# Performance work log

Measured on AMD Instinct MI355X. Metric: run time of the kernel, lower is better.

## Reference

```python
import jax, jax.numpy as jnp
import numpy as np

HIDDEN = 2048
N_HEADS = 16
N_KV_HEADS = 4
HEAD_DIM = 128
N_REP = N_HEADS // N_KV_HEADS
BATCH = 2
SEQ = 2048
SCALE = HEAD_DIM ** -0.5
NEG = -1e9


def apply_rope(x, freqs):
    # x: (b, s, h, d); freqs: (s, d//2) angles. Interleaved-pair rotation.
    cos = jnp.cos(freqs)[None, :, None, :]
    sin = jnp.sin(freqs)[None, :, None, :]
    x1 = x[..., 0::2]
    x2 = x[..., 1::2]
    r1 = x1 * cos - x2 * sin
    r2 = x1 * sin + x2 * cos
    return jnp.stack([r1, r2], axis=-1).reshape(x.shape)


def setup_inputs() -> dict:
    key = jax.random.key(0)
    ks = jax.random.split(key, 6)
    x = jax.random.normal(ks[0], (BATCH, SEQ, HIDDEN), dtype=jnp.float32)
    wq = jax.random.normal(ks[1], (N_HEADS * HEAD_DIM, HIDDEN), dtype=jnp.float32) * 0.02
    wk = jax.random.normal(ks[2], (N_KV_HEADS * HEAD_DIM, HIDDEN), dtype=jnp.float32) * 0.02
    wv = jax.random.normal(ks[3], (N_KV_HEADS * HEAD_DIM, HIDDEN), dtype=jnp.float32) * 0.02
    wo = jax.random.normal(ks[4], (HIDDEN, N_HEADS * HEAD_DIM), dtype=jnp.float32) * 0.02
    # RoPE angle table: pos * theta^{-2i/d}
    inv_freq = 1.0 / (10000.0 ** (jnp.arange(0, HEAD_DIM, 2, dtype=jnp.float32) / HEAD_DIM))
    rope_freqs = jnp.arange(SEQ, dtype=jnp.float32)[:, None] * inv_freq[None, :]  # (S, d/2)
    # additive causal mask
    causal = jnp.tril(jnp.ones((SEQ, SEQ), dtype=bool))
    mask = jnp.where(causal, 0.0, NEG).astype(jnp.float32)[None, None]  # (1,1,S,S)
    return {"x": x, "wq": wq, "wk": wk, "wv": wv, "wo": wo,
            "rope_freqs": rope_freqs, "mask": mask}


def reference(x, wq, wk, wv, wo, rope_freqs, mask):
    b, s, _ = x.shape
    q = (x @ wq.T).reshape(b, s, N_HEADS, HEAD_DIM)
    k = (x @ wk.T).reshape(b, s, N_KV_HEADS, HEAD_DIM)
    v = (x @ wv.T).reshape(b, s, N_KV_HEADS, HEAD_DIM)
    q = apply_rope(q, rope_freqs)
    k = apply_rope(k, rope_freqs)
    new_k, new_v = k, v  # kv cache (no prior cache, start_pos=0)
    # GQA: repeat each kv head n_rep times (matches expand+reshape in source)
    k_rep = jnp.repeat(k, N_REP, axis=2)  # (b, s, n_heads, d)
    v_rep = jnp.repeat(v, N_REP, axis=2)
    scores = jnp.einsum('bqhd,bkhd->bhqk', q, k_rep) * SCALE
    scores = scores + mask
    attn = jax.nn.softmax(scores.astype(jnp.float32), axis=-1).astype(q.dtype)
    out = jnp.einsum('bhqk,bkhd->bqhd', attn, v_rep).reshape(b, s, -1)
    return out @ wo.T, (new_k, new_v)
```

## Files before the change

### kernel.cpp

```cpp
#include <hip/hip_runtime.h>
#include <hip/hip_bf16.h>

#define NH 16
#define NKV 4
#define HD 128
#define QSCALE 0.1275174272f

using bf16x8 = __attribute__((ext_vector_type(8))) __bf16;
using f32x4  = __attribute__((ext_vector_type(4))) float;
using u16x8  = __attribute__((ext_vector_type(8))) unsigned short;
using u16x4  = __attribute__((ext_vector_type(4))) unsigned short;
using u16x2  = __attribute__((ext_vector_type(2))) unsigned short;

__device__ __forceinline__ unsigned short f2b(float f) {
  __hip_bfloat16 h = __float2bfloat16(f);
  return __builtin_bit_cast(unsigned short, h);
}
__device__ __forceinline__ float b2f(unsigned short u) {
  unsigned int v = ((unsigned int)u) << 16;
  return __builtin_bit_cast(float, v);
}

__device__ __forceinline__ void glds16(const unsigned short* g, unsigned short* l) {
  __builtin_amdgcn_global_load_lds(
      (const __attribute__((address_space(1))) unsigned int*)(const void*)g,
      (__attribute__((address_space(3))) unsigned int*)(void*)l, 16, 0, 0);
}

__global__ __launch_bounds__(256) void cvt_fused(const float* __restrict__ x,
                                                 const float* __restrict__ wq,
                                                 const float* __restrict__ wk,
                                                 const float* __restrict__ wv,
                                                 const float* __restrict__ wo,
                                                 const float* __restrict__ freqs,
                                                 unsigned short* __restrict__ xb,
                                                 unsigned short* __restrict__ wqkvb,
                                                 unsigned short* __restrict__ wob,
                                                 float2* __restrict__ cs_tab) {
  int i = blockIdx.x * 256 + threadIdx.x;
  if (i >= 2359296) {
    int k = i - 2359296;
    float f = freqs[k];
    float2 cs; cs.x = cosf(f); cs.y = sinf(f);
    cs_tab[k] = cs;
    return;
  }
  const float* src;
  unsigned short* dst;
  int off;
  if (i < 1048576)      { src = x;  dst = xb;              off = i; }
  else if (i < 1572864) { src = wq; dst = wqkvb;           off = i - 1048576; }
  else if (i < 1703936) { src = wk; dst = wqkvb + 4194304; off = i - 1572864; }
  else if (i < 1835008) { src = wv; dst = wqkvb + 5242880; off = i - 1703936; }
  else                  { src = wo; dst = wob;             off = i - 1835008; }
  const float4* s4 = reinterpret_cast<const float4*>(src) + (size_t)off * 2;
  float4 v0 = s4[0], v1 = s4[1];
  u16x8 o;
  o[0] = f2b(v0.x); o[1] = f2b(v0.y); o[2] = f2b(v0.z); o[3] = f2b(v0.w);
  o[4] = f2b(v1.x); o[5] = f2b(v1.y); o[6] = f2b(v1.z); o[7] = f2b(v1.w);
  reinterpret_cast<u16x8*>(dst)[off] = o;
}

__global__ __launch_bounds__(512, 1) void gemm_qkv(const unsigned short* __restrict__ A,
                                                   const unsigned short* __restrict__ B,
                                                   const float2* __restrict__ cs_tab,
                                                   unsigned short* __restrict__ qro,
                                                   unsigned short* __restrict__ kro,
                                                   unsigned short* __restrict__ vt,
                                                   float* __restrict__ newk,
                                                   float* __restrict__ newv,
                                                   int K) {
  constexpr int BN = 384;
  constexpr int AF = 4, BF = 6, BH = 3, BL = 3;
  __shared__ unsigned short As[3][128 * 32];
  __shared__ unsigned short Bs[3][BN * 32];
  const int tid = threadIdx.x, lane = tid & 63;
  const int wid = tid >> 6, wm = wid >> 2, wn = wid & 3;
  const int cpx = gridDim.x >> 3;
  const int wgid = (blockIdx.x & 7) * cpx + (blockIdx.x >> 3);
  const int bx = wgid % 8, by = wgid / 8;
  const int row0 = by * 128, col0 = bx * BN;
  const int fr = lane & 15, g = lane >> 4;
  const int NT = K >> 5;

  size_t offA;
  {
    int cid = tid, R = cid >> 3, phys = cid & 7, cl = phys ^ (R & 7);
    offA = (size_t)(row0 + 2 * R + (cl >> 2)) * K + (cl & 3) * 8;
  }
  size_t offB[BL];
#pragma unroll
  for (int l = 0; l < BL; l++) {
    int cid = tid + l * 512, R = cid >> 3, phys = cid & 7, cl = phys ^ (R & 7);
    offB[l] = (size_t)(col0 + 2 * R + (cl >> 2)) * K + (cl & 3) * 8;
  }

  auto stage_p0 = [&](int t, int sb) {
    int k0 = t * 32;
    glds16(A + offA + k0, &As[sb][tid * 8]);
    glds16(B + offB[0] + k0, &Bs[sb][tid * 8]);
  };
  auto stage_p1 = [&](int t, int sb) {
    int k0 = t * 32;
#pragma unroll
    for (int l = 1; l < BL; l++)
      glds16(B + offB[l] + k0, &Bs[sb][(tid + l * 512) * 8]);
  };

  auto ldfrag = [&](const unsigned short* buf, int row) {
    int R = row >> 1;
    int phys = ((((row & 1) << 2) | g) ^ (R & 7));
    return *reinterpret_cast<const bf16x8*>(&buf[R * 64 + phys * 8]);
  };

  f32x4 acc[AF][BF];
#pragma unroll
  for (int i = 0; i < AF; i++)
#pragma unroll
    for (int j = 0; j < BF; j++) acc[i][j] = f32x4{0.f, 0.f, 0.f, 0.f};

  stage_p0(0, 0); stage_p1(0, 0);
  stage_p0(1, 1); stage_p1(1, 1);
  asm volatile("s_waitcnt vmcnt(4)" ::: "memory");
  __builtin_amdgcn_s_barrier();
  __builtin_amdgcn_sched_barrier(0);

  int rb = 0, sb = 2;
#pragma unroll 1
  for (int t = 0; t < NT; ++t) {
    const unsigned short* Ar = &As[rb][0];
    const unsigned short* Br = &Bs[rb][0];

    bf16x8 af[AF], bfr[BF];
#pragma unroll
    for (int mf = 0; mf < AF; mf++) af[mf] = ldfrag(Ar, wm * 64 + mf * 16 + fr);
#pragma unroll
    for (int nf = 0; nf < BH; nf++) bfr[nf] = ldfrag(Br, wn * 96 + nf * 16 + fr);
    if (t + 2 < NT) stage_p0(t + 2, sb);
    __builtin_amdgcn_s_barrier();
    asm volatile("s_waitcnt lgkmcnt(0)" ::: "memory");
    __builtin_amdgcn_sched_barrier(0);
    __builtin_amdgcn_s_setprio(1);
#pragma unroll
    for (int mf = 0; mf < AF; mf++)
#pragma unroll
      for (int nf = 0; nf < BH; nf++)
        acc[mf][nf] = __builtin_amdgcn_mfma_f32_16x16x32_bf16(af[mf], bfr[nf], acc[mf][nf], 0, 0, 0);
    __builtin_amdgcn_s_setprio(0);
    __builtin_amdgcn_sched_barrier(0);
    __builtin_amdgcn_s_barrier();

#pragma unroll
    for (int nf = BH; nf < BF; nf++) bfr[nf] = ldfrag(Br, wn * 96 + nf * 16 + fr);
    if (t + 2 < NT) stage_p1(t + 2, sb);
    __builtin_amdgcn_s_barrier();
    asm volatile("s_waitcnt lgkmcnt(0)" ::: "memory");
    __builtin_amdgcn_sched_barrier(0);
    __builtin_amdgcn_s_setprio(1);
#pragma unroll
    for (int mf = 0; mf < AF; mf++)
#pragma unroll
      for (int nf = BH; nf < BF; nf++)
        acc[mf][nf] = __builtin_amdgcn_mfma_f32_16x16x32_bf16(af[mf], bfr[nf], acc[mf][nf], 0, 0, 0);
    __builtin_amdgcn_s_setprio(0);
    __builtin_amdgcn_sched_barrier(0);

    if (t + 1 < NT) {
      if (t + 2 < NT) asm volatile("s_waitcnt vmcnt(4)" ::: "memory");
      else            asm volatile("s_waitcnt vmcnt(0)" ::: "memory");
      __builtin_amdgcn_s_barrier();
      __builtin_amdgcn_sched_barrier(0);
    }
    rb = rb == 2 ? 0 : rb + 1;
    sb = sb == 2 ? 0 : sb + 1;
  }

#pragma unroll
  for (int i = 0; i < AF; i++) {
    int rbase = row0 + wm * 64 + i * 16 + g * 4;
    int bb = rbase >> 11;
    int sr0 = rbase & 2047;
#pragma unroll
    for (int j = 0; j < BF; j++) {
      int cb = col0 + wn * 96 + j * 16 + fr;
      int d = cb & 127;
      if (cb < 2048) {
        int hq = cb >> 7;
        unsigned short* qp = qro + ((size_t)(bb * 16 + hq) * 2048 + sr0) * 128 + d;
#pragma unroll
        for (int r = 0; r < 4; r++) {
          float own = acc[i][j][r];
          float par = __shfl_xor(own, 1);
          float2 cs = cs_tab[(sr0 + r) * 64 + (d >> 1)];
          float o = (fr & 1) ? (par * cs.y + own * cs.x) : (own * cs.x - par * cs.y);
          qp[(size_t)r * 128] = f2b(o * QSCALE);
        }
      } else if (cb < 2560) {
        int kvh = (cb >> 7) & 3;
        unsigned short* kp = kro + ((size_t)(bb * 4 + kvh) * 2048 + sr0) * 128 + d;
        float* nk = newk + ((size_t)bb * 2048 + sr0) * 512 + kvh * 128 + d;
#pragma unroll
        for (int r = 0; r < 4; r++) {
          float own = acc[i][j][r];
          float par = __shfl_xor(own, 1);
          float2 cs = cs_tab[(sr0 + r) * 64 + (d >> 1)];
          float o = (fr & 1) ? (par * cs.y + own * cs.x) : (own * cs.x - par * cs.y);
          kp[(size_t)r * 128] = f2b(o);
          nk[(size_t)r * 512] = o;
        }
      } else {
        int kvh = (cb >> 7) & 3;
        float* nv = newv + ((size_t)bb * 2048 + sr0) * 512 + kvh * 128 + d;
        u16x4 pack;
#pragma unroll
        for (int r = 0; r < 4; r++) {
          float v = acc[i][j][r];
          nv[(size_t)r * 512] = v;
          pack[r] = f2b(v);
        }
        int kl = sr0 & 31;
        int slotb = ((kl >> 2) & 3) * 8 + (kl >> 4) * 4;
        *reinterpret_cast<u16x4*>(vt + ((size_t)(bb * 4 + kvh) * 128 + d) * 2048
                                  + (sr0 & ~31) + slotb) = pack;
      }
    }
  }
}

template<int CF32, int BN>
__global__ __launch_bounds__(512, 1) void gemm_full(const unsigned short* __restrict__ A,
                                                    const unsigned short* __restrict__ B,
                                                    void* __restrict__ C,
                                                    int N, int K, int nbx) {
  constexpr int BM = 128;
  constexpr int AF = 4;
  constexpr int BF = BN / 64;
  constexpr int BH = BF / 2;
  constexpr int AL = 1;
  constexpr int BL = BN / 128;
  __shared__ unsigned short As[3][BM * 32];
  __shared__ unsigned short Bs[3][BN * 32];
  const int tid = threadIdx.x, lane = tid & 63;
  const int wid = tid >> 6, wm = wid >> 2, wn = wid & 3;
  const int cpx = gridDim.x >> 3;
  const int wgid = (blockIdx.x & 7) * cpx + (blockIdx.x >> 3);
  const int bx = wgid % nbx, by = wgid / nbx;
  const int row0 = by * BM, col0 = bx * BN;
  const int fr = lane & 15, g = lane >> 4;
  const int NT = K >> 5;

  size_t offA;
  {
    int cid = tid, R = cid >> 3, phys = cid & 7, cl = phys ^ (R & 7);
    offA = (size_t)(row0 + 2 * R + (cl >> 2)) * K + (cl & 3) * 8;
  }
  size_t offB[BL];
#pragma unroll
  for (int l = 0; l < BL; l++) {
    int cid = tid + l * 512, R = cid >> 3, phys = cid & 7, cl = phys ^ (R & 7);
    offB[l] = (size_t)(col0 + 2 * R + (cl >> 2)) * K + (cl & 3) * 8;
  }

  auto stage_p0 = [&](int t, int sb) {
    int k0 = t * 32;
    glds16(A + offA + k0, &As[sb][tid * 8]);
    glds16(B + offB[0] + k0, &Bs[sb][tid * 8]);
  };
  auto stage_p1 = [&](int t, int sb) {
    int k0 = t * 32;
#pragma unroll
    for (int l = 1; l < BL; l++)
      glds16(B + offB[l] + k0, &Bs[sb][(tid + l * 512) * 8]);
  };

  auto ldfrag = [&](const unsigned short* buf, int row) {
    int R = row >> 1;
    int phys = ((((row & 1) << 2) | g) ^ (R & 7));
    return *reinterpret_cast<const bf16x8*>(&buf[R * 64 + phys * 8]);
  };

  f32x4 acc[AF][BF];
#pragma unroll
  for (int i = 0; i < AF; i++)
#pragma unroll
    for (int j = 0; j < BF; j++) acc[i][j] = f32x4{0.f, 0.f, 0.f, 0.f};

  stage_p0(0, 0); stage_p1(0, 0);
  stage_p0(1, 1); stage_p1(1, 1);
  if constexpr (AL + BL == 4) asm volatile("s_waitcnt vmcnt(4)" ::: "memory");
  else                        asm volatile("s_waitcnt vmcnt(3)" ::: "memory");
  __builtin_amdgcn_s_barrier();
  __builtin_amdgcn_sched_barrier(0);

  int rb = 0, sb = 2;
#pragma unroll 1
  for (int t = 0; t < NT; ++t) {
    const unsigned short* Ar = &As[rb][0];
    const unsigned short* Br = &Bs[rb][0];

    bf16x8 af[AF], bfr[BF];
#pragma unroll
    for (int mf = 0; mf < AF; mf++) af[mf] = ldfrag(Ar, wm * 64 + mf * 16 + fr);
#pragma unroll
    for (int nf = 0; nf < BH; nf++) bfr[nf] = ldfrag(Br, wn * (BN / 4) + nf * 16 + fr);
    if (t + 2 < NT) stage_p0(t + 2, sb);
    __builtin_amdgcn_s_barrier();
    asm volatile("s_waitcnt lgkmcnt(0)" ::: "memory");
    __builtin_amdgcn_sched_barrier(0);
    __builtin_amdgcn_s_setprio(1);
#pragma unroll
    for (int mf = 0; mf < AF; mf++)
#pragma unroll
      for (int nf = 0; nf < BH; nf++)
        acc[mf][nf] = __builtin_amdgcn_mfma_f32_16x16x32_bf16(af[mf], bfr[nf], acc[mf][nf], 0, 0, 0);
    __builtin_amdgcn_s_setprio(0);
    __builtin_amdgcn_sched_barrier(0);
    __builtin_amdgcn_s_barrier();

#pragma unroll
    for (int nf = BH; nf < BF; nf++) bfr[nf] = ldfrag(Br, wn * (BN / 4) + nf * 16 + fr);
    if (t + 2 < NT) stage_p1(t + 2, sb);
    __builtin_amdgcn_s_barrier();
    asm volatile("s_waitcnt lgkmcnt(0)" ::: "memory");
    __builtin_amdgcn_sched_barrier(0);
    __builtin_amdgcn_s_setprio(1);
#pragma unroll
    for (int mf = 0; mf < AF; mf++)
#pragma unroll
      for (int nf = BH; nf < BF; nf++)
        acc[mf][nf] = __builtin_amdgcn_mfma_f32_16x16x32_bf16(af[mf], bfr[nf], acc[mf][nf], 0, 0, 0);
    __builtin_amdgcn_s_setprio(0);
    __builtin_amdgcn_sched_barrier(0);

    if (t + 1 < NT) {
      if (t + 2 < NT) {
        if constexpr (AL + BL == 4) asm volatile("s_waitcnt vmcnt(4)" ::: "memory");
        else                        asm volatile("s_waitcnt vmcnt(3)" ::: "memory");
      } else {
        asm volatile("s_waitcnt vmcnt(0)" ::: "memory");
      }
      __builtin_amdgcn_s_barrier();
      __builtin_amdgcn_sched_barrier(0);
    }
    rb = rb == 2 ? 0 : rb + 1;
    sb = sb == 2 ? 0 : sb + 1;
  }

#pragma unroll
  for (int i = 0; i < AF; i++) {
#pragma unroll
    for (int j = 0; j < BF; j++) {
      int rbase = row0 + wm * 64 + i * 16 + g * 4;
      int cb = col0 + wn * (BN / 4) + j * 16 + fr;
#pragma unroll
      for (int r = 0; r < 4; r++) {
        if (CF32)
          reinterpret_cast<float*>(C)[(size_t)(rbase + r) * N + cb] = acc[i][j][r];
        else
          reinterpret_cast<unsigned short*>(C)[(size_t)(rbase + r) * N + cb] = f2b(acc[i][j][r]);
      }
    }
  }
}

__global__ __launch_bounds__(512, 4) void attn_kernel(const unsigned short* __restrict__ qro,
                                                      const unsigned short* __restrict__ kro,
                                                      const unsigned short* __restrict__ vt,
                                                      unsigned short* __restrict__ out) {
  __shared__ unsigned short Ks[2][32 * 128];
  __shared__ unsigned short Vs[2][64 * 64];
  const int tid = threadIdx.x, lane = tid & 63, w = tid >> 6;
  const int kvhb = blockIdx.x & 7;
  const int kvh = kvhb & 3, b = kvhb >> 2;
  const int s = blockIdx.x >> 3;
  const int T = (s < 32) ? s : (95 - s);
  const int sub = w >> 2, hh = w & 3;
  const int h = kvh * 4 + hh;
  const int qbase = T * 32 + sub * 16;
  const int fr = lane & 15, g = lane >> 4, fk = g * 8;
  const unsigned short* Kp = kro + (size_t)(b * 4 + kvh) * 2048 * 128;
  const unsigned short* Vtp = vt + (size_t)(b * 4 + kvh) * 128 * 2048;
  const unsigned short* Qp = qro + ((size_t)(b * 16 + h) * 2048 + qbase) * 128;

  bf16x8 qf[4];
#pragma unroll
  for (int kk = 0; kk < 4; kk++)
    qf[kk] = *reinterpret_cast<const bf16x8*>(Qp + fr * 128 + kk * 32 + fk);

  u16x8 onesu;
#pragma unroll
  for (int j = 0; j < 8; j++) onesu[j] = 0x3F80;
  bf16x8 ones = __builtin_bit_cast(bf16x8, onesu);

  f32x4 o[8];
#pragma unroll
  for (int dt = 0; dt < 8; dt++) o[dt] = f32x4{0.f, 0.f, 0.f, 0.f};
  f32x4 dacc = f32x4{0.f, 0.f, 0.f, 0.f};
  const int qrow_s = qbase + fr;
  const int niter = T + 1;

  const int krow = w * 4 + (lane >> 4);
  const int kcol = lane & 15;
  const int vr = w * 8 + (lane >> 3);
  const int vcol = lane & 7;

  auto stage = [&](int kv0, int buf) {
    glds16(Kp + (size_t)(kv0 + krow) * 128 + ((kcol ^ (krow & 7)) * 8),
           &Ks[buf][w * 4 * 128]);
    int u = vcol ^ (vr & 7);
    int d = 2 * vr + (u >> 2);
    glds16(Vtp + (size_t)d * 2048 + kv0 + (u & 3) * 8,
           &Vs[buf][w * 8 * 64]);
  };

  auto step = [&](int kv0, bool mask, int buf) {
    const unsigned short* Kb = &Ks[buf][0];
    const unsigned short* Vb = &Vs[buf][0];
    f32x4 sc[2];
    sc[0] = sc[1] = f32x4{0.f, 0.f, 0.f, 0.f};
    __builtin_amdgcn_s_setprio(1);
#pragma unroll
    for (int kk = 0; kk < 4; kk++) {
      int blk = ((kk * 4 + g) ^ (fr & 7)) * 8;
      bf16x8 ka0 = *reinterpret_cast<const bf16x8*>(Kb + (fr +  0) * 128 + blk);
      bf16x8 ka1 = *reinterpret_cast<const bf16x8*>(Kb + (fr + 16) * 128 + blk);
      sc[0] = __builtin_amdgcn_mfma_f32_16x16x32_bf16(ka0, qf[kk], sc[0], 0, 0, 0);
      sc[1] = __builtin_amdgcn_mfma_f32_16x16x32_bf16(ka1, qf[kk], sc[1], 0, 0, 0);
    }
    __builtin_amdgcn_s_setprio(0);
#pragma unroll
    for (int ss = 0; ss < 2; ss++)
#pragma unroll
      for (int r = 0; r < 4; r++) {
        float v = sc[ss][r];
        if (mask && (kv0 + 16 * ss + 4 * g + r > qrow_s)) v = -1e30f;
        sc[ss][r] = __builtin_amdgcn_exp2f(v);
      }
    u16x8 pau;
#pragma unroll
    for (int j = 0; j < 4; j++) {
      pau[j]     = f2b(sc[0][j]);
      pau[4 + j] = f2b(sc[1][j]);
    }
    bf16x8 pa = __builtin_bit_cast(bf16x8, pau);
    dacc = __builtin_amdgcn_mfma_f32_16x16x32_bf16(pa, ones, dacc, 0, 0, 0);
    __builtin_amdgcn_s_setprio(1);
#pragma unroll
    for (int dt = 0; dt < 8; dt++) {
      int jr = dt * 8 + (fr >> 1);
      int c = ((fr & 1) * 4 + g) ^ (fr >> 1);
      bf16x8 vf = *reinterpret_cast<const bf16x8*>(Vb + jr * 64 + c * 8);
      o[dt] = __builtin_amdgcn_mfma_f32_16x16x32_bf16(pa, vf, o[dt], 0, 0, 0);
    }
    __builtin_amdgcn_s_setprio(0);
  };

  stage(0, 0);
  int buf = 0;
  for (int i = 0; i < niter; i++) {
    __syncthreads();
    if (i + 1 < niter) stage((i + 1) * 32, buf ^ 1);
    step(i * 32, i == niter - 1, buf);
    buf ^= 1;
  }

#pragma unroll
  for (int r = 0; r < 4; r++) {
    float inv = 1.0f / dacc[r];
    int qrow = qbase + g * 4 + r;
    size_t rowoff = ((size_t)b * 2048 + qrow) * 2048 + (size_t)h * 128;
#pragma unroll
    for (int dt = 0; dt < 8; dt++)
      out[rowoff + dt * 16 + fr] = f2b(o[dt][r] * inv);
  }
}

extern "C" void kernel_launch(void* const* d_in, const int* in_sizes, int n_in,
                              void* d_out, int out_size, void* d_ws, size_t ws_size,
                              hipStream_t stream) {
  const float* x  = (const float*)d_in[0];
  const float* wq = (const float*)d_in[1];
  const float* wk = (const float*)d_in[2];
  const float* wv = (const float*)d_in[3];
  const float* wo = (const float*)d_in[4];
  const float* freqs = (const float*)d_in[5];

  char* ws = (char*)d_ws;
  unsigned short* xb    = (unsigned short*)(ws);
  unsigned short* attn  = xb;
  unsigned short* wqkvb = (unsigned short*)(ws + 16777216);
  unsigned short* wob   = (unsigned short*)(ws + 29360128);
  float2*         cstab = (float2*)(ws + 37748736);
  unsigned short* qro   = (unsigned short*)(ws + 62914560);
  unsigned short* kro   = (unsigned short*)(ws + 79691776);
  unsigned short* vt    = (unsigned short*)(ws + 83886080);

  float* out_o = (float*)d_out;
  float* out_k = (float*)d_out + 8388608;
  float* out_v = (float*)d_out + 10485760;

  cvt_fused<<<9728, 256, 0, stream>>>(x, wq, wk, wv, wo, freqs, xb, wqkvb, wob, cstab);

  gemm_qkv<<<256, 512, 0, stream>>>(xb, wqkvb, cstab, qro, kro, vt, out_k, out_v, 2048);

  attn_kernel<<<512, 512, 0, stream>>>(qro, kro, vt, attn);

  gemm_full<1, 256><<<256, 512, 0, stream>>>(attn, wob, out_o, 2048, 2048, 8);
}
```

Baseline: 195.4 us.

## Replace large-tile triple-buffered GEMMs with 128x128 double-buffered tiles and more blocks

Both the QKV projection and output projection GEMMs drop their 128x384/128x256 tiles with 512 threads, triple buffering and hand-tuned waitcnt/barrier splitting. They now use 128x128 tiles with 256 threads, simple double buffering and __syncthreads, launching 768 and 512 blocks with up to 3 blocks per CU. The aim is higher occupancy and better CU load balance across the grid. In exchange, per-block operand reuse drops, the finer-grained latency hiding schedule is gone, and more global traffic is needed per output.

Measured after the change: 193.1 us. About the same (-1.2%).

```diff
diff --git a/kernel.cpp b/kernel.cpp
--- a/kernel.cpp
+++ b/kernel.cpp
@@ -61,7 +61,31 @@
   reinterpret_cast<u16x8*>(dst)[off] = o;
 }
 
-__global__ __launch_bounds__(512, 1) void gemm_qkv(const unsigned short* __restrict__ A,
+
+#define GEMM97_PREAMBLE(Kvar)                                                  \
+  const int tid = threadIdx.x, lane = tid & 63;                                \
+  const int wid = tid >> 6, wm = wid >> 1, wn = wid & 1;                       \
+  const int cpx = gridDim.x >> 3;                                              \
+  const int wgid = (blockIdx.x & 7) * cpx + (blockIdx.x >> 3);                 \
+  const int bx = wgid % nbx, by = wgid / nbx;                                  \
+  const int row0 = by * 128, col0 = bx * 128;                                  \
+  const int fr = lane & 15, g = lane >> 4;                                     \
+  const int NT = (Kvar) >> 5;                                                  \
+  size_t offA[2], offB[2];                                                     \
+  _Pragma("unroll")                                                            \
+  for (int l = 0; l < 2; l++) {                                                \
+    int cid = tid + l * 256, R = cid >> 3, phys = cid & 7, cl = phys ^ (R & 7);\
+    offA[l] = (size_t)(row0 + 2 * R + (cl >> 2)) * (Kvar) + (cl & 3) * 8;      \
+    offB[l] = (size_t)(col0 + 2 * R + (cl >> 2)) * (Kvar) + (cl & 3) * 8;      \
+  }
+
+__device__ __forceinline__ bf16x8 ldfrag97(const unsigned short* buf, int row, int g) {
+  int R = row >> 1;
+  int phys = ((((row & 1) << 2) | g) ^ (R & 7));
+  return *reinterpret_cast<const bf16x8*>(&buf[R * 64 + phys * 8]);
+}
+
+__global__ __launch_bounds__(256, 3) void gemm_qkv(const unsigned short* __restrict__ A,
                                                    const unsigned short* __restrict__ B,
                                                    const float2* __restrict__ cs_tab,
                                                    unsigned short* __restrict__ qro,
@@ -69,120 +93,55 @@
                                                    unsigned short* __restrict__ vt,
                                                    float* __restrict__ newk,
                                                    float* __restrict__ newv,
-                                                   int K) {
-  constexpr int BN = 384;
-  constexpr int AF = 4, BF = 6, BH = 3, BL = 3;
-  __shared__ unsigned short As[3][128 * 32];
-  __shared__ unsigned short Bs[3][BN * 32];
-  const int tid = threadIdx.x, lane = tid & 63;
-  const int wid = tid >> 6, wm = wid >> 2, wn = wid & 3;
-  const int cpx = gridDim.x >> 3;
-  const int wgid = (blockIdx.x & 7) * cpx + (blockIdx.x >> 3);
-  const int bx = wgid % 8, by = wgid / 8;
-  const int row0 = by * 128, col0 = bx * BN;
-  const int fr = lane & 15, g = lane >> 4;
-  const int NT = K >> 5;
-
-  size_t offA;
-  {
-    int cid = tid, R = cid >> 3, phys = cid & 7, cl = phys ^ (R & 7);
-    offA = (size_t)(row0 + 2 * R + (cl >> 2)) * K + (cl & 3) * 8;
-  }
-  size_t offB[BL];
-#pragma unroll
-  for (int l = 0; l < BL; l++) {
-    int cid = tid + l * 512, R = cid >> 3, phys = cid & 7, cl = phys ^ (R & 7);
-    offB[l] = (size_t)(col0 + 2 * R + (cl >> 2)) * K + (cl & 3) * 8;
-  }
-
-  auto stage_p0 = [&](int t, int sb) {
+                                                   int K, int nbx) {
+  __shared__ unsigned short As[2][128 * 32];
+  __shared__ unsigned short Bs[2][128 * 32];
+  GEMM97_PREAMBLE(K)
+
+  auto stage = [&](int t, int sb) {
     int k0 = t * 32;
-    glds16(A + offA + k0, &As[sb][tid * 8]);
-    glds16(B + offB[0] + k0, &Bs[sb][tid * 8]);
+#pragma unroll
+    for (int l = 0; l < 2; l++) {
+      glds16(A + offA[l] + k0, &As[sb][(tid + l * 256) * 8]);
+      glds16(B + offB[l] + k0, &Bs[sb][(tid + l * 256) * 8]);
+    }
   };
-  auto stage_p1 = [&](int t, int sb) {
-    int k0 = t * 32;
-#pragma unroll
-    for (int l = 1; l < BL; l++)
-      glds16(B + offB[l] + k0, &Bs[sb][(tid + l * 512) * 8]);
-  };
-
-  auto ldfrag = [&](const unsigned short* buf, int row) {
-    int R = row >> 1;
-    int phys = ((((row & 1) << 2) | g) ^ (R & 7));
-    return *reinterpret_cast<const bf16x8*>(&buf[R * 64 + phys * 8]);
-  };
-
-  f32x4 acc[AF][BF];
-#pragma unroll
-  for (int i = 0; i < AF; i++)
-#pragma unroll
-    for (int j = 0; j < BF; j++) acc[i][j] = f32x4{0.f, 0.f, 0.f, 0.f};
-
-  stage_p0(0, 0); stage_p1(0, 0);
-  stage_p0(1, 1); stage_p1(1, 1);
-  asm volatile("s_waitcnt vmcnt(4)" ::: "memory");
-  __builtin_amdgcn_s_barrier();
-  __builtin_amdgcn_sched_barrier(0);
-
-  int rb = 0, sb = 2;
+
+  f32x4 acc[4][4];
+#pragma unroll
+  for (int i = 0; i < 4; i++)
+#pragma unroll
+    for (int j = 0; j < 4; j++) acc[i][j] = f32x4{0.f, 0.f, 0.f, 0.f};
+
+  stage(0, 0);
+  int buf = 0;
 #pragma unroll 1
   for (int t = 0; t < NT; ++t) {
-    const unsigned short* Ar = &As[rb][0];
-    const unsigned short* Br = &Bs[rb][0];
-
-    bf16x8 af[AF], bfr[BF];
-#pragma unroll
-    for (int mf = 0; mf < AF; mf++) af[mf] = ldfrag(Ar, wm * 64 + mf * 16 + fr);
-#pragma unroll
-    for (int nf = 0; nf < BH; nf++) bfr[nf] = ldfrag(Br, wn * 96 + nf * 16 + fr);
-    if (t + 2 < NT) stage_p0(t + 2, sb);
-    __builtin_amdgcn_s_barrier();
-    asm volatile("s_waitcnt lgkmcnt(0)" ::: "memory");
-    __builtin_amdgcn_sched_barrier(0);
+    __syncthreads();
+    if (t + 1 < NT) stage(t + 1, buf ^ 1);
+    bf16x8 af[4], bfr[4];
+#pragma unroll
+    for (int mf = 0; mf < 4; mf++) af[mf] = ldfrag97(As[buf], wm * 64 + mf * 16 + fr, g);
+#pragma unroll
+    for (int nf = 0; nf < 4; nf++) bfr[nf] = ldfrag97(Bs[buf], wn * 64 + nf * 16 + fr, g);
     __builtin_amdgcn_s_setprio(1);
 #pragma unroll
-    for (int mf = 0; mf < AF; mf++)
-#pragma unroll
-      for (int nf = 0; nf < BH; nf++)
+    for (int mf = 0; mf < 4; mf++)
+#pragma unroll
+      for (int nf = 0; nf < 4; nf++)
         acc[mf][nf] = __builtin_amdgcn_mfma_f32_16x16x32_bf16(af[mf], bfr[nf], acc[mf][nf], 0, 0, 0);
     __builtin_amdgcn_s_setprio(0);
-    __builtin_amdgcn_sched_barrier(0);
-    __builtin_amdgcn_s_barrier();
-
-#pragma unroll
-    for (int nf = BH; nf < BF; nf++) bfr[nf] = ldfrag(Br, wn * 96 + nf * 16 + fr);
-    if (t + 2 < NT) stage_p1(t + 2, sb);
-    __builtin_amdgcn_s_barrier();
-    asm volatile("s_waitcnt lgkmcnt(0)" ::: "memory");
-    __builtin_amdgcn_sched_barrier(0);
-    __builtin_amdgcn_s_setprio(1);
-#pragma unroll
-    for (int mf = 0; mf < AF; mf++)
-#pragma unroll
-      for (int nf = BH; nf < BF; nf++)
-        acc[mf][nf] = __builtin_amdgcn_mfma_f32_16x16x32_bf16(af[mf], bfr[nf], acc[mf][nf], 0, 0, 0);
-    __builtin_amdgcn_s_setprio(0);
-    __builtin_amdgcn_sched_barrier(0);
-
-    if (t + 1 < NT) {
-      if (t + 2 < NT) asm volatile("s_waitcnt vmcnt(4)" ::: "memory");
-      else            asm volatile("s_waitcnt vmcnt(0)" ::: "memory");
-      __builtin_amdgcn_s_barrier();
-      __builtin_amdgcn_sched_barrier(0);
-    }
-    rb = rb == 2 ? 0 : rb + 1;
-    sb = sb == 2 ? 0 : sb + 1;
-  }
-
-#pragma unroll
-  for (int i = 0; i < AF; i++) {
+    buf ^= 1;
+  }
+
+#pragma unroll
+  for (int i = 0; i < 4; i++) {
     int rbase = row0 + wm * 64 + i * 16 + g * 4;
     int bb = rbase >> 11;
     int sr0 = rbase & 2047;
 #pragma unroll
-    for (int j = 0; j < BF; j++) {
-      int cb = col0 + wn * 96 + j * 16 + fr;
+    for (int j = 0; j < 4; j++) {
+      int cb = col0 + wn * 64 + j * 16 + fr;
       int d = cb & 127;
       if (cb < 2048) {
         int hq = cb >> 7;
@@ -227,138 +186,59 @@
   }
 }
 
-template<int CF32, int BN>
-__global__ __launch_bounds__(512, 1) void gemm_full(const unsigned short* __restrict__ A,
-                                                    const unsigned short* __restrict__ B,
-                                                    void* __restrict__ C,
-                                                    int N, int K, int nbx) {
-  constexpr int BM = 128;
-  constexpr int AF = 4;
-  constexpr int BF = BN / 64;
-  constexpr int BH = BF / 2;
-  constexpr int AL = 1;
-  constexpr int BL = BN / 128;
-  __shared__ unsigned short As[3][BM * 32];
-  __shared__ unsigned short Bs[3][BN * 32];
-  const int tid = threadIdx.x, lane = tid & 63;
-  const int wid = tid >> 6, wm = wid >> 2, wn = wid & 3;
-  const int cpx = gridDim.x >> 3;
-  const int wgid = (blockIdx.x & 7) * cpx + (blockIdx.x >> 3);
-  const int bx = wgid % nbx, by = wgid / nbx;
-  const int row0 = by * BM, col0 = bx * BN;
-  const int fr = lane & 15, g = lane >> 4;
-  const int NT = K >> 5;
-
-  size_t offA;
-  {
-    int cid = tid, R = cid >> 3, phys = cid & 7, cl = phys ^ (R & 7);
-    offA = (size_t)(row0 + 2 * R + (cl >> 2)) * K + (cl & 3) * 8;
-  }
-  size_t offB[BL];
-#pragma unroll
-  for (int l = 0; l < BL; l++) {
-    int cid = tid + l * 512, R = cid >> 3, phys = cid & 7, cl = phys ^ (R & 7);
-    offB[l] = (size_t)(col0 + 2 * R + (cl >> 2)) * K + (cl & 3) * 8;
-  }
-
-  auto stage_p0 = [&](int t, int sb) {
+__global__ __launch_bounds__(256, 3) void gemm_o(const unsigned short* __restrict__ A,
+                                                 const unsigned short* __restrict__ B,
+                                                 float* __restrict__ C,
+                                                 int N, int K, int nbx) {
+  __shared__ unsigned short As[2][128 * 32];
+  __shared__ unsigned short Bs[2][128 * 32];
+  GEMM97_PREAMBLE(K)
+
+  auto stage = [&](int t, int sb) {
     int k0 = t * 32;
-    glds16(A + offA + k0, &As[sb][tid * 8]);
-    glds16(B + offB[0] + k0, &Bs[sb][tid * 8]);
+#pragma unroll
+    for (int l = 0; l < 2; l++) {
+      glds16(A + offA[l] + k0, &As[sb][(tid + l * 256) * 8]);
+      glds16(B + offB[l] + k0, &Bs[sb][(tid + l * 256) * 8]);
+    }
   };
-  auto stage_p1 = [&](int t, int sb) {
-    int k0 = t * 32;
-#pragma unroll
-    for (int l = 1; l < BL; l++)
-      glds16(B + offB[l] + k0, &Bs[sb][(tid + l * 512) * 8]);
-  };
-
-  auto ldfrag = [&](const unsigned short* buf, int row) {
-    int R = row >> 1;
-    int phys = ((((row & 1) << 2) | g) ^ (R & 7));
-    return *reinterpret_cast<const bf16x8*>(&buf[R * 64 + phys * 8]);
-  };
-
-  f32x4 acc[AF][BF];
-#pragma unroll
-  for (int i = 0; i < AF; i++)
-#pragma unroll
-    for (int j = 0; j < BF; j++) acc[i][j] = f32x4{0.f, 0.f, 0.f, 0.f};
-
-  stage_p0(0, 0); stage_p1(0, 0);
-  stage_p0(1, 1); stage_p1(1, 1);
-  if constexpr (AL + BL == 4) asm volatile("s_waitcnt vmcnt(4)" ::: "memory");
-  else                        asm volatile("s_waitcnt vmcnt(3)" ::: "memory");
-  __builtin_amdgcn_s_barrier();
-  __builtin_amdgcn_sched_barrier(0);
-
-  int rb = 0, sb = 2;
+
+  f32x4 acc[4][4];
+#pragma unroll
+  for (int i = 0; i < 4; i++)
+#pragma unroll
+    for (int j = 0; j < 4; j++) acc[i][j] = f32x4{0.f, 0.f, 0.f, 0.f};
+
+  stage(0, 0);
+  int buf = 0;
 #pragma unroll 1
   for (int t = 0; t < NT; ++t) {
-    const unsigned short* Ar = &As[rb][0];
-    const unsigned short* Br = &Bs[rb][0];
-
-    bf16x8 af[AF], bfr[BF];
-#pragma unroll
-    for (int mf = 0; mf < AF; mf++) af[mf] = ldfrag(Ar, wm * 64 + mf * 16 + fr);
-#pragma unroll
-    for (int nf = 0; nf < BH; nf++) bfr[nf] = ldfrag(Br, wn * (BN / 4) + nf * 16 + fr);
-    if (t + 2 < NT) stage_p0(t + 2, sb);
-    __builtin_amdgcn_s_barrier();
-    asm volatile("s_waitcnt lgkmcnt(0)" ::: "memory");
-    __builtin_amdgcn_sched_barrier(0);
+    __syncthreads();
+    if (t + 1 < NT) stage(t + 1, buf ^ 1);
+    bf16x8 af[4], bfr[4];
+#pragma unroll
+    for (int mf = 0; mf < 4; mf++) af[mf] = ldfrag97(As[buf], wm * 64 + mf * 16 + fr, g);
+#pragma unroll
+    for (int nf = 0; nf < 4; nf++) bfr[nf] = ldfrag97(Bs[buf], wn * 64 + nf * 16 + fr, g);
     __builtin_amdgcn_s_setprio(1);
 #pragma unroll
-    for (int mf = 0; mf < AF; mf++)
-#pragma unroll
-      for (int nf = 0; nf < BH; nf++)
+    for (int mf = 0; mf < 4; mf++)
+#pragma unroll
+      for (int nf = 0; nf < 4; nf++)
         acc[mf][nf] = __builtin_amdgcn_mfma_f32_16x16x32_bf16(af[mf], bfr[nf], acc[mf][nf], 0, 0, 0);
     __builtin_amdgcn_s_setprio(0);
-    __builtin_amdgcn_sched_barrier(0);
-    __builtin_amdgcn_s_barrier();
-
-#pragma unroll
-    for (int nf = BH; nf < BF; nf++) bfr[nf] = ldfrag(Br, wn * (BN / 4) + nf * 16 + fr);
-    if (t + 2 < NT) stage_p1(t + 2, sb);
-    __builtin_amdgcn_s_barrier();
-    asm volatile("s_waitcnt lgkmcnt(0)" ::: "memory");
-    __builtin_amdgcn_sched_barrier(0);
-    __builtin_amdgcn_s_setprio(1);
-#pragma unroll
-    for (int mf = 0; mf < AF; mf++)
-#pragma unroll
-      for (int nf = BH; nf < BF; nf++)
-        acc[mf][nf] = __builtin_amdgcn_mfma_f32_16x16x32_bf16(af[mf], bfr[nf], acc[mf][nf], 0, 0, 0);
-    __builtin_amdgcn_s_setprio(0);
-    __builtin_amdgcn_sched_barrier(0);
-
-    if (t + 1 < NT) {
-      if (t + 2 < NT) {
-        if constexpr (AL + BL == 4) asm volatile("s_waitcnt vmcnt(4)" ::: "memory");
-        else                        asm volatile("s_waitcnt vmcnt(3)" ::: "memory");
-      } else {
-        asm volatile("s_waitcnt vmcnt(0)" ::: "memory");
-      }
-      __builtin_amdgcn_s_barrier();
-      __builtin_amdgcn_sched_barrier(0);
-    }
-    rb = rb == 2 ? 0 : rb + 1;
-    sb = sb == 2 ? 0 : sb + 1;
-  }
-
-#pragma unroll
-  for (int i = 0; i < AF; i++) {
-#pragma unroll
-    for (int j = 0; j < BF; j++) {
+    buf ^= 1;
+  }
+
+#pragma unroll
+  for (int i = 0; i < 4; i++) {
+#pragma unroll
+    for (int j = 0; j < 4; j++) {
       int rbase = row0 + wm * 64 + i * 16 + g * 4;
-      int cb = col0 + wn * (BN / 4) + j * 16 + fr;
-#pragma unroll
-      for (int r = 0; r < 4; r++) {
-        if (CF32)
-          reinterpret_cast<float*>(C)[(size_t)(rbase + r) * N + cb] = acc[i][j][r];
-        else
-          reinterpret_cast<unsigned short*>(C)[(size_t)(rbase + r) * N + cb] = f2b(acc[i][j][r]);
-      }
+      int cb = col0 + wn * 64 + j * 16 + fr;
+#pragma unroll
+      for (int r = 0; r < 4; r++)
+        C[(size_t)(rbase + r) * N + cb] = acc[i][j][r];
     }
   }
 }
@@ -501,9 +381,9 @@
 
   cvt_fused<<<9728, 256, 0, stream>>>(x, wq, wk, wv, wo, freqs, xb, wqkvb, wob, cstab);
 
-  gemm_qkv<<<256, 512, 0, stream>>>(xb, wqkvb, cstab, qro, kro, vt, out_k, out_v, 2048);
+  gemm_qkv<<<768, 256, 0, stream>>>(xb, wqkvb, cstab, qro, kro, vt, out_k, out_v, 2048, 24);
 
   attn_kernel<<<512, 512, 0, stream>>>(qro, kro, vt, attn);
 
-  gemm_full<1, 256><<<256, 512, 0, stream>>>(attn, wob, out_o, 2048, 2048, 8);
-}
+  gemm_o<<<512, 256, 0, stream>>>(attn, wob, out_o, 2048, 2048, 16);
+}
```
